# Performance work log

Hardware: AMD Instinct MI355X
Metric: run time of the kernel (lower is better)

Reference implementation:

```python
import jax, jax.numpy as jnp
import numpy as np

TAU = 10.0 / 7.0
V_TH = 1.0
ALPHA = 10.0  # sigmoid surrogate slope

@jax.custom_vjp
def spike_fn(v):
    # Heaviside(v - v_th) forward, sigmoid surrogate backward
    return (v >= V_TH).astype(v.dtype)

def _spike_fwd(v):
    return spike_fn(v), v

def _spike_bwd(v, g):
    s = jax.nn.sigmoid(ALPHA * (v - V_TH))
    return (g * ALPHA * s * (1.0 - s),)

spike_fn.defvjp(_spike_fwd, _spike_bwd)

def lif_multistep(x_bctm):
    # x: [B, C, T, M]; LIF recurrence over T axis, v_reset=0 hard reset,
    # decay_input=True: v = v + (x - v)/tau
    x_t = jnp.moveaxis(x_bctm, 2, 0)  # [T, B, C, M]
    def step(v, x):
        v = v + (x - v) / TAU
        s = spike_fn(v)
        v = v * (1.0 - s)  # hard reset to 0 (not detached)
        return v, s
    v0 = jnp.zeros_like(x_t[0])
    _, s_t = jax.lax.scan(step, v0, x_t)
    return jnp.moveaxis(s_t, 0, 2)  # [B, C, T, M]

def conv2d(x, w, pad, dil):
    return jax.lax.conv_general_dilated(
        x, w, window_strides=(1, 1),
        padding=[(pad[0], pad[0]), (pad[1], pad[1])],
        rhs_dilation=dil,
        dimension_numbers=('NCHW', 'OIHW', 'NCHW'))

def setup_inputs() -> dict:
    key = jax.random.key(0)
    k0, k1, k2, k3, k4 = jax.random.split(key, 5)
    B, T, M = 32, 128, 40
    x = jax.random.normal(k0, (B, 1, T, M), dtype=jnp.float32)
    # kaiming-ish init: std = 1/sqrt(fan_in)
    w1 = jax.random.normal(k1, (64, 1, 4, 3), dtype=jnp.float32) / np.sqrt(1 * 4 * 3)
    w2 = jax.random.normal(k2, (64, 64, 4, 3), dtype=jnp.float32) / np.sqrt(64 * 4 * 3)
    w3 = jax.random.normal(k3, (64, 64, 4, 3), dtype=jnp.float32) / np.sqrt(64 * 4 * 3)
    kw, kb = jax.random.split(k4)
    wf = jax.random.normal(kw, (12, 64 * 40), dtype=jnp.float32) / np.sqrt(64 * 40)
    bf = jnp.zeros((12,), dtype=jnp.float32)
    return {"x": x, "w1": w1, "w2": w2, "w3": w3, "wf": wf, "bf": bf}

def reference(x, w1, w2, w3, wf, bf):
    h = conv2d(x, w1, (2, 1), (1, 1))     # [B,64,T+1,40]
    h = lif_multistep(h)
    h = conv2d(h, w2, (6, 3), (4, 3))     # shape preserved
    h = lif_multistep(h)
    h = conv2d(h, w3, (24, 9), (16, 9))   # shape preserved
    h = lif_multistep(h)
    B, C, T, M = h.shape
    h = jnp.transpose(h, (0, 2, 1, 3)).reshape(B, T, C * M)  # flatten=True path
    y = h @ wf.T + bf                     # [B, T, 12]
    return y.mean(axis=1)                 # [B, 12]
```

## Files before the change

kernel.cpp:

```cpp
#include <hip/hip_runtime.h>


typedef __attribute__((ext_vector_type(8))) _Float16 v8h;
typedef __attribute__((ext_vector_type(16))) float v16f;
typedef __attribute__((ext_vector_type(4))) unsigned int u32x4;
typedef _Float16 half_t;

#define NB 32
#define NC 64
#define NT 129
#define TIN 128
#define NM 40
#define MS8 72
#define ROWB8 2952
#define SROWB8 2560

__global__ void prep_conv1(const float* __restrict__ w2s, const float* __restrict__ w3s,
                           uint4* __restrict__ wf2o, uint4* __restrict__ wf3o,
                           const float* __restrict__ x, const float* __restrict__ w1,
                           unsigned char* __restrict__ s1) {
    const int bx = blockIdx.x;
    if (bx < 96) {
        const float* w = (bx < 48) ? w2s : w3s;
        uint4* wf = (bx < 48) ? wf2o : wf3o;
        int tid = (bx % 48) * 256 + threadIdx.x;
        int lane = tid & 63;
        int rest = tid >> 6;
        int hl = rest & 1;
        int ct = (rest >> 1) & 1;
        int cq = (rest >> 2) & 3;
        int tap = rest >> 4;
        int kh = tap / 3, kw = tap % 3;
        int co = ct * 32 + (lane & 31);
        unsigned short o[8];
#pragma unroll
        for (int jj = 0; jj < 8; jj++) {
            int ci = cq * 16 + (lane >> 5) * 8 + jj;
            float wv = w[((co * 64 + ci) * 4 + kh) * 3 + kw];
            _Float16 hi = (_Float16)wv;
            _Float16 val = hl ? (_Float16)((wv - (float)hi) * 2048.0f) : hi;
            unsigned short us;
            __builtin_memcpy(&us, &val, 2);
            o[jj] = us;
        }
        uint4 r;
        __builtin_memcpy(&r, o, 16);
        wf[tid] = r;
        return;
    }
    const int idx = bx - 96;
    const int mg = idx % 10;
    const int b = idx / 10;
    const int c = threadIdx.x & 63;
    const int ml = threadIdx.x >> 6;
    const int m = mg * 4 + ml;
    float w[4][3];
#pragma unroll
    for (int kh = 0; kh < 4; kh++)
#pragma unroll
        for (int kw = 0; kw < 3; kw++) w[kh][kw] = w1[(c * 4 + kh) * 3 + kw];
    const float* xb = x + (size_t)b * TIN * NM;

    float xw[12][3];
#pragma unroll
    for (int rr = 0; rr < 12; rr++)
#pragma unroll
        for (int kw = 0; kw < 3; kw++) xw[rr][kw] = 0.f;
#pragma unroll
    for (int rr = 2; rr < 4; rr++)
#pragma unroll
        for (int kw = 0; kw < 3; kw++) {
            int mc = m - 1 + kw;
            xw[rr][kw] = ((unsigned)mc < (unsigned)NM) ? xb[(rr - 2) * NM + mc] : 0.f;
        }

    unsigned char* orow = s1 + ((size_t)b * NT * NM + m) * 64 + c;
    float v = 0.f;
    const float TAUc = 10.0f / 7.0f;

    for (int tb = 0; tb < NT; tb += 8) {
#pragma unroll
        for (int q = 0; q < 8; q++) {
            int row = tb + 2 + q;
#pragma unroll
            for (int kw = 0; kw < 3; kw++) {
                int mc = m - 1 + kw;
                xw[4 + q][kw] = (row < TIN && (unsigned)mc < (unsigned)NM)
                                    ? xb[row * NM + mc] : 0.f;
            }
        }
        int kmax = (NT - tb) < 8 ? (NT - tb) : 8;
#pragma unroll
        for (int k = 0; k < 8; k++) {
            if (k < kmax) {
                float uacc = 0.f;
#pragma unroll
                for (int kh = 0; kh < 4; kh++)
#pragma unroll
                    for (int kw = 0; kw < 3; kw++) uacc += xw[k + kh][kw] * w[kh][kw];
                v = v + (uacc - v) / TAUc;
                orow[(size_t)(tb + k) * NM * 64] = (v >= 1.0f) ? 1 : 0;
                if (v >= 1.0f) v = 0.0f;
            }
        }
#pragma unroll
        for (int rr = 0; rr < 4; rr++)
#pragma unroll
            for (int kw = 0; kw < 3; kw++) xw[rr][kw] = xw[8 + rr][kw];
    }
}

__device__ inline unsigned mul3c00(unsigned x) {
    unsigned r;
    asm("v_mul_u32_u24 %0, 0x3C00, %1" : "=v"(r) : "v"(x));
    return r;
}

__device__ inline v8h expand01(uint2 raw) {
    unsigned o0 = mul3c00(__builtin_amdgcn_perm(0u, raw.x, 0x04010400u));
    unsigned o1 = mul3c00(__builtin_amdgcn_perm(0u, raw.x, 0x04030402u));
    unsigned o2 = mul3c00(__builtin_amdgcn_perm(0u, raw.y, 0x04010400u));
    unsigned o3 = mul3c00(__builtin_amdgcn_perm(0u, raw.y, 0x04030402u));
    uint4 o = make_uint4(o0, o1, o2, o3);
    return __builtin_bit_cast(v8h, o);
}

template <int DH, int PH, int DW, int PW, int RMOD>
__global__ __launch_bounds__(256, 2) void convW(const unsigned char* __restrict__ spk,
                                                const uint4* __restrict__ wfrag,
                                                float* __restrict__ u) {
    __shared__ uint2 ldsq[7 * ROWB8 / 8];
    char* lds = (char*)ldsq;
    const int tid = threadIdx.x;
    const int lane = tid & 63;
    const int wv = tid >> 6;
    const int wp = wv >> 1;
    const int hl = wv & 1;
    const int bx = blockIdx.x;
    const int b = blockIdx.y;
    int r, jj0;
    if (bx < 32) { r = bx % RMOD; jj0 = (bx / RMOD) * 4; }
    else         { r = 0;         jj0 = (32 / RMOD) * 4; }

    const char* spb = (const char*)spk + (size_t)b * NT * SROWB8;
#pragma unroll
    for (int k = 0; k < 9; k++) {
        int c = tid + k * 256;
        if (c < 2296) {
            int i = c / 328;
            int rem = c - i * 328;
            int s = rem >> 3;
            int q = rem & 7;
            int tg = r - PH + DH * (jj0 + i);
            uint2 val = make_uint2(0u, 0u);
            if ((unsigned)tg < (unsigned)NT && s < 40)
                val = *(const uint2*)(spb + ((size_t)tg * NM + s) * 64 + q * 8);
            *(uint2*)(lds + i * ROWB8 + s * MS8 + q * 8) = val;
        }
    }

    const int pos = lane & 31;
    const int jl = pos >> 4;
    const int ml = pos & 15;
    const int hseg = lane >> 5;
    const int jj = jj0 + 2 * wp + jl;
    const int ldsrow = 2 * wp + jl;
    const int t = r + DH * jj;
    const int mtb[3] = {0, 16, 24};

    int P[3][3];
#pragma unroll
    for (int mt = 0; mt < 3; mt++)
#pragma unroll
        for (int kw = 0; kw < 3; kw++) {
            int md = mtb[mt] + ml + kw * DW - PW;
            int sel = ((unsigned)md < 40u) ? md : 40;
            P[mt][kw] = ldsrow * ROWB8 + sel * MS8 + hseg * 8;
        }

    v16f acc[3][2];
#pragma unroll
    for (int a = 0; a < 3; a++)
#pragma unroll
        for (int c2 = 0; c2 < 2; c2++) acc[a][c2] = (v16f)(0.0f);

    unsigned voff0 = (unsigned)(hl * 1024 + lane * 16);
    unsigned voff1 = voff0 + 4096u;
    const char* wbp = (const char*)wfrag;
    u32x4 Ab[2][4];

#define ISSUE4(PAR)                                                                   \
    {                                                                                 \
        asm volatile("global_load_dwordx4 %0, %1, %2"                                 \
                     : "=v"(Ab[PAR][0]) : "v"(voff0), "s"(wbp));                      \
        asm volatile("global_load_dwordx4 %0, %1, %2 offset:2048"                     \
                     : "=v"(Ab[PAR][1]) : "v"(voff0), "s"(wbp));                      \
        asm volatile("global_load_dwordx4 %0, %1, %2"                                 \
                     : "=v"(Ab[PAR][2]) : "v"(voff1), "s"(wbp));                      \
        asm volatile("global_load_dwordx4 %0, %1, %2 offset:2048"                     \
                     : "=v"(Ab[PAR][3]) : "v"(voff1), "s"(wbp));                      \
        wbp += 8192;                                                                  \
    }

    ISSUE4(0);
    __syncthreads();

#pragma unroll
    for (int s = 0; s < 24; ++s) {
        const int tap = s >> 1;
        const int kh = tap / 3, kw = tap % 3;
        if (s < 23) {
            if ((s & 1) == 0) ISSUE4(1) else ISSUE4(0);
            asm volatile("s_waitcnt vmcnt(4)");
        } else {
            asm volatile("s_waitcnt vmcnt(0)");
        }
        __builtin_amdgcn_sched_barrier(0);
#pragma unroll
        for (int j = 0; j < 2; ++j) {
            const int cq = (s & 1) * 2 + j;
            uint2 r0 = *(const uint2*)(lds + P[0][kw] + kh * ROWB8 + cq * 16);
            uint2 r1 = *(const uint2*)(lds + P[1][kw] + kh * ROWB8 + cq * 16);
            uint2 r2 = *(const uint2*)(lds + P[2][kw] + kh * ROWB8 + cq * 16);
            v8h B0 = expand01(r0);
            v8h B1 = expand01(r1);
            v8h B2 = expand01(r2);
            v8h A0 = __builtin_bit_cast(v8h, Ab[s & 1][j * 2 + 0]);
            v8h A1 = __builtin_bit_cast(v8h, Ab[s & 1][j * 2 + 1]);
            acc[0][0] = __builtin_amdgcn_mfma_f32_32x32x16_f16(A0, B0, acc[0][0], 0, 0, 0);
            acc[0][1] = __builtin_amdgcn_mfma_f32_32x32x16_f16(A1, B0, acc[0][1], 0, 0, 0);
            acc[1][0] = __builtin_amdgcn_mfma_f32_32x32x16_f16(A0, B1, acc[1][0], 0, 0, 0);
            acc[1][1] = __builtin_amdgcn_mfma_f32_32x32x16_f16(A1, B1, acc[1][1], 0, 0, 0);
            acc[2][0] = __builtin_amdgcn_mfma_f32_32x32x16_f16(A0, B2, acc[2][0], 0, 0, 0);
            acc[2][1] = __builtin_amdgcn_mfma_f32_32x32x16_f16(A1, B2, acc[2][1], 0, 0, 0);
        }
    }
#undef ISSUE4

    const float invs = 1.0f / 2048.0f;
    float4* lred = (float4*)lds;
    __syncthreads();
#pragma unroll
    for (int mt = 0; mt < 3; mt++) {
        if (hl) {
#pragma unroll
            for (int ct = 0; ct < 2; ct++)
#pragma unroll
                for (int g = 0; g < 4; g++) {
                    float4 vv;
                    vv.x = acc[mt][ct][4 * g + 0];
                    vv.y = acc[mt][ct][4 * g + 1];
                    vv.z = acc[mt][ct][4 * g + 2];
                    vv.w = acc[mt][ct][4 * g + 3];
                    lred[(wp * 8 + ct * 4 + g) * 64 + lane] = vv;
                }
        }
        __syncthreads();
        if (!hl && t < NT) {
            int m = mtb[mt] + ml;
            float* base = u + ((size_t)(b * NT + t) * NM + m) * 64;
#pragma unroll
            for (int ct = 0; ct < 2; ct++)
#pragma unroll
                for (int g = 0; g < 4; g++) {
                    float4 lo = lred[(wp * 8 + ct * 4 + g) * 64 + lane];
                    int co = ct * 32 + 8 * g + 4 * hseg;
                    float4 val;
                    val.x = acc[mt][ct][4 * g + 0] + lo.x * invs;
                    val.y = acc[mt][ct][4 * g + 1] + lo.y * invs;
                    val.z = acc[mt][ct][4 * g + 2] + lo.z * invs;
                    val.w = acc[mt][ct][4 * g + 3] + lo.w * invs;
                    *(float4*)(base + co) = val;
                }
        }
        __syncthreads();
    }
}

__global__ void lif_spikes(const float* __restrict__ u, unsigned char* __restrict__ s2) {
    int tid = blockIdx.x * 256 + threadIdx.x;
    int b = tid / 2560;
    int cm = tid % 2560;
    const float* up = u + (size_t)b * NT * 2560 + cm;
    unsigned char* sp = s2 + (size_t)b * NT * 2560 + cm;
    float v = 0.f;
    const float TAUc = 10.0f / 7.0f;
    for (int tb = 0; tb < 128; tb += 16) {
        float uu[16];
#pragma unroll
        for (int k = 0; k < 16; k++) uu[k] = up[(size_t)(tb + k) * 2560];
#pragma unroll
        for (int k = 0; k < 16; k++) {
            v = v + (uu[k] - v) / TAUc;
            sp[(size_t)(tb + k) * 2560] = (v >= 1.0f) ? 1 : 0;
            if (v >= 1.0f) v = 0.f;
        }
    }
    float uu = up[(size_t)128 * 2560];
    v = v + (uu - v) / TAUc;
    sp[(size_t)128 * 2560] = (v >= 1.0f) ? 1 : 0;
}

__global__ void lif_sum(const float* __restrict__ u, float* __restrict__ hsum) {
    int tid = blockIdx.x * 256 + threadIdx.x;
    int b = tid / 2560;
    int cm = tid % 2560;
    int m = cm >> 6;
    int co = cm & 63;
    const float* up = u + (size_t)b * NT * 2560 + cm;
    float v = 0.f, cnt = 0.f;
    const float TAUc = 10.0f / 7.0f;
    for (int tb = 0; tb < 128; tb += 16) {
        float uu[16];
#pragma unroll
        for (int k = 0; k < 16; k++) uu[k] = up[(size_t)(tb + k) * 2560];
#pragma unroll
        for (int k = 0; k < 16; k++) {
            v = v + (uu[k] - v) / TAUc;
            if (v >= 1.0f) { cnt += 1.0f; v = 0.f; }
        }
    }
    float uu = up[(size_t)128 * 2560];
    v = v + (uu - v) / TAUc;
    if (v >= 1.0f) cnt += 1.0f;
    hsum[b * 2560 + co * NM + m] = cnt;
}

__global__ void fc_out(const float* __restrict__ hsum, const float* __restrict__ wf,
                       const float* __restrict__ bfv, float* __restrict__ out) {
    int b = blockIdx.x;
    int tid = threadIdx.x;
    float p[12];
#pragma unroll
    for (int k = 0; k < 12; k++) p[k] = 0.0f;
    for (int cm = tid; cm < NC * NM; cm += 256) {
        float h = hsum[b * NC * NM + cm];
#pragma unroll
        for (int k = 0; k < 12; k++) p[k] += h * wf[k * (NC * NM) + cm];
    }
    __shared__ float red[12][4];
    int lane = tid & 63, w = tid >> 6;
#pragma unroll
    for (int k = 0; k < 12; k++) {
        float s = p[k];
#pragma unroll
        for (int off = 32; off > 0; off >>= 1) s += __shfl_down(s, off, 64);
        if (lane == 0) red[k][w] = s;
    }
    __syncthreads();
    if (tid < 12) {
        float s = red[tid][0] + red[tid][1] + red[tid][2] + red[tid][3];
        out[b * 12 + tid] = bfv[tid] + s / 129.0f;
    }
}

extern "C" void kernel_launch(void* const* d_in, const int* in_sizes, int n_in,
                              void* d_out, int out_size, void* d_ws, size_t ws_size,
                              hipStream_t stream) {
    const float* x  = (const float*)d_in[0];
    const float* w1 = (const float*)d_in[1];
    const float* w2 = (const float*)d_in[2];
    const float* w3 = (const float*)d_in[3];
    const float* wf = (const float*)d_in[4];
    const float* bf = (const float*)d_in[5];
    float* out = (float*)d_out;

    char* ws = (char*)d_ws;
    unsigned char* s1 = (unsigned char*)ws;
    unsigned char* s2 = (unsigned char*)(ws + 10567680);
    float*  u   = (float*)(ws + 21135360);
    uint4*  wf2 = (uint4*)(ws + 63406080);
    uint4*  wf3 = (uint4*)(ws + 63602688);
    float* hsum = (float*)(ws + 63799296);

    prep_conv1<<<416, 256, 0, stream>>>(w2, w3, wf2, wf3, x, w1, s1);

    convW<4, 6, 3, 3, 4><<<dim3(33, 32), 256, 0, stream>>>(s1, wf2, u);
    lif_spikes<<<320, 256, 0, stream>>>(u, s2);

    convW<16, 24, 9, 9, 16><<<dim3(33, 32), 256, 0, stream>>>(s2, wf3, u);
    lif_sum<<<320, 256, 0, stream>>>(u, hsum);

    fc_out<<<32, 256, 0, stream>>>(hsum, wf, bf, out);
}
```

Baseline: 201.8 us.

## Split conv work across output-channel halves per wave, doubling block count

Each block now covers two output time rows instead of four. The four waves are split by output-channel half (32 channels each) and by input-channel half, instead of by row pair. Per-wave accumulators shrink from six to three MFMA tiles, LDS use drops from 7 to 5 rows, and launch bounds rise to 4 blocks per CU, with twice as many blocks in the grid. The aim is higher occupancy and better load balance. In exchange, the spike-row halo is reloaded more often relative to the work done, and each B fragment is reused by fewer MFMAs.

```diff
diff --git a/kernel.cpp b/kernel.cpp
--- a/kernel.cpp
+++ b/kernel.cpp
@@ -126,27 +126,27 @@
 }
 
 template <int DH, int PH, int DW, int PW, int RMOD>
-__global__ __launch_bounds__(256, 2) void convW(const unsigned char* __restrict__ spk,
+__global__ __launch_bounds__(256, 4) void convW(const unsigned char* __restrict__ spk,
                                                 const uint4* __restrict__ wfrag,
                                                 float* __restrict__ u) {
-    __shared__ uint2 ldsq[7 * ROWB8 / 8];
+    __shared__ uint2 ldsq[5 * ROWB8 / 8];
     char* lds = (char*)ldsq;
     const int tid = threadIdx.x;
     const int lane = tid & 63;
     const int wv = tid >> 6;
-    const int wp = wv >> 1;
+    const int ct = wv >> 1;
     const int hl = wv & 1;
     const int bx = blockIdx.x;
     const int b = blockIdx.y;
     int r, jj0;
-    if (bx < 32) { r = bx % RMOD; jj0 = (bx / RMOD) * 4; }
-    else         { r = 0;         jj0 = (32 / RMOD) * 4; }
+    if (bx < 64) { r = bx % RMOD; jj0 = (bx / RMOD) * 2; }
+    else         { r = 0;         jj0 = (64 / RMOD) * 2; }
 
     const char* spb = (const char*)spk + (size_t)b * NT * SROWB8;
 #pragma unroll
-    for (int k = 0; k < 9; k++) {
+    for (int k = 0; k < 7; k++) {
         int c = tid + k * 256;
-        if (c < 2296) {
+        if (c < 1640) {
             int i = c / 328;
             int rem = c - i * 328;
             int s = rem >> 3;
@@ -163,8 +163,8 @@
     const int jl = pos >> 4;
     const int ml = pos & 15;
     const int hseg = lane >> 5;
-    const int jj = jj0 + 2 * wp + jl;
-    const int ldsrow = 2 * wp + jl;
+    const int jj = jj0 + jl;
+    const int ldsrow = jl;
     const int t = r + DH * jj;
     const int mtb[3] = {0, 16, 24};
 
@@ -178,31 +178,25 @@
             P[mt][kw] = ldsrow * ROWB8 + sel * MS8 + hseg * 8;
         }
 
-    v16f acc[3][2];
-#pragma unroll
-    for (int a = 0; a < 3; a++)
-#pragma unroll
-        for (int c2 = 0; c2 < 2; c2++) acc[a][c2] = (v16f)(0.0f);
-
-    unsigned voff0 = (unsigned)(hl * 1024 + lane * 16);
+    v16f acc[3];
+#pragma unroll
+    for (int a = 0; a < 3; a++) acc[a] = (v16f)(0.0f);
+
+    unsigned voff0 = (unsigned)(ct * 2048 + hl * 1024 + lane * 16);
     unsigned voff1 = voff0 + 4096u;
     const char* wbp = (const char*)wfrag;
-    u32x4 Ab[2][4];
-
-#define ISSUE4(PAR)                                                                   \
+    u32x4 Ab[2][2];
+
+#define ISSUE2(PAR)                                                                   \
     {                                                                                 \
         asm volatile("global_load_dwordx4 %0, %1, %2"                                 \
                      : "=v"(Ab[PAR][0]) : "v"(voff0), "s"(wbp));                      \
-        asm volatile("global_load_dwordx4 %0, %1, %2 offset:2048"                     \
-                     : "=v"(Ab[PAR][1]) : "v"(voff0), "s"(wbp));                      \
         asm volatile("global_load_dwordx4 %0, %1, %2"                                 \
-                     : "=v"(Ab[PAR][2]) : "v"(voff1), "s"(wbp));                      \
-        asm volatile("global_load_dwordx4 %0, %1, %2 offset:2048"                     \
-                     : "=v"(Ab[PAR][3]) : "v"(voff1), "s"(wbp));                      \
+                     : "=v"(Ab[PAR][1]) : "v"(voff1), "s"(wbp));                      \
         wbp += 8192;                                                                  \
     }
 
-    ISSUE4(0);
+    ISSUE2(0);
     __syncthreads();
 
 #pragma unroll
@@ -210,8 +204,8 @@
         const int tap = s >> 1;
         const int kh = tap / 3, kw = tap % 3;
         if (s < 23) {
-            if ((s & 1) == 0) ISSUE4(1) else ISSUE4(0);
-            asm volatile("s_waitcnt vmcnt(4)");
+            if ((s & 1) == 0) ISSUE2(1) else ISSUE2(0);
+            asm volatile("s_waitcnt vmcnt(2)");
         } else {
             asm volatile("s_waitcnt vmcnt(0)");
         }
@@ -225,17 +219,13 @@
             v8h B0 = expand01(r0);
             v8h B1 = expand01(r1);
             v8h B2 = expand01(r2);
-            v8h A0 = __builtin_bit_cast(v8h, Ab[s & 1][j * 2 + 0]);
-            v8h A1 = __builtin_bit_cast(v8h, Ab[s & 1][j * 2 + 1]);
-            acc[0][0] = __builtin_amdgcn_mfma_f32_32x32x16_f16(A0, B0, acc[0][0], 0, 0, 0);
-            acc[0][1] = __builtin_amdgcn_mfma_f32_32x32x16_f16(A1, B0, acc[0][1], 0, 0, 0);
-            acc[1][0] = __builtin_amdgcn_mfma_f32_32x32x16_f16(A0, B1, acc[1][0], 0, 0, 0);
-            acc[1][1] = __builtin_amdgcn_mfma_f32_32x32x16_f16(A1, B1, acc[1][1], 0, 0, 0);
-            acc[2][0] = __builtin_amdgcn_mfma_f32_32x32x16_f16(A0, B2, acc[2][0], 0, 0, 0);
-            acc[2][1] = __builtin_amdgcn_mfma_f32_32x32x16_f16(A1, B2, acc[2][1], 0, 0, 0);
-        }
-    }
-#undef ISSUE4
+            v8h A = __builtin_bit_cast(v8h, Ab[s & 1][j]);
+            acc[0] = __builtin_amdgcn_mfma_f32_32x32x16_f16(A, B0, acc[0], 0, 0, 0);
+            acc[1] = __builtin_amdgcn_mfma_f32_32x32x16_f16(A, B1, acc[1], 0, 0, 0);
+            acc[2] = __builtin_amdgcn_mfma_f32_32x32x16_f16(A, B2, acc[2], 0, 0, 0);
+        }
+    }
+#undef ISSUE2
 
     const float invs = 1.0f / 2048.0f;
     float4* lred = (float4*)lds;
@@ -244,34 +234,30 @@
     for (int mt = 0; mt < 3; mt++) {
         if (hl) {
 #pragma unroll
-            for (int ct = 0; ct < 2; ct++)
-#pragma unroll
-                for (int g = 0; g < 4; g++) {
-                    float4 vv;
-                    vv.x = acc[mt][ct][4 * g + 0];
-                    vv.y = acc[mt][ct][4 * g + 1];
-                    vv.z = acc[mt][ct][4 * g + 2];
-                    vv.w = acc[mt][ct][4 * g + 3];
-                    lred[(wp * 8 + ct * 4 + g) * 64 + lane] = vv;
-                }
+            for (int g = 0; g < 4; g++) {
+                float4 vv;
+                vv.x = acc[mt][4 * g + 0];
+                vv.y = acc[mt][4 * g + 1];
+                vv.z = acc[mt][4 * g + 2];
+                vv.w = acc[mt][4 * g + 3];
+                lred[(ct * 4 + g) * 64 + lane] = vv;
+            }
         }
         __syncthreads();
         if (!hl && t < NT) {
             int m = mtb[mt] + ml;
             float* base = u + ((size_t)(b * NT + t) * NM + m) * 64;
 #pragma unroll
-            for (int ct = 0; ct < 2; ct++)
-#pragma unroll
-                for (int g = 0; g < 4; g++) {
-                    float4 lo = lred[(wp * 8 + ct * 4 + g) * 64 + lane];
-                    int co = ct * 32 + 8 * g + 4 * hseg;
-                    float4 val;
-                    val.x = acc[mt][ct][4 * g + 0] + lo.x * invs;
-                    val.y = acc[mt][ct][4 * g + 1] + lo.y * invs;
-                    val.z = acc[mt][ct][4 * g + 2] + lo.z * invs;
-                    val.w = acc[mt][ct][4 * g + 3] + lo.w * invs;
-                    *(float4*)(base + co) = val;
-                }
+            for (int g = 0; g < 4; g++) {
+                float4 lo = lred[(ct * 4 + g) * 64 + lane];
+                int co = ct * 32 + 8 * g + 4 * hseg;
+                float4 val;
+                val.x = acc[mt][4 * g + 0] + lo.x * invs;
+                val.y = acc[mt][4 * g + 1] + lo.y * invs;
+                val.z = acc[mt][4 * g + 2] + lo.z * invs;
+                val.w = acc[mt][4 * g + 3] + lo.w * invs;
+                *(float4*)(base + co) = val;
+            }
         }
         __syncthreads();
     }
@@ -375,10 +361,10 @@
 
     prep_conv1<<<416, 256, 0, stream>>>(w2, w3, wf2, wf3, x, w1, s1);
 
-    convW<4, 6, 3, 3, 4><<<dim3(33, 32), 256, 0, stream>>>(s1, wf2, u);
+    convW<4, 6, 3, 3, 4><<<dim3(65, 32), 256, 0, stream>>>(s1, wf2, u);
     lif_spikes<<<320, 256, 0, stream>>>(u, s2);
 
-    convW<16, 24, 9, 9, 16><<<dim3(33, 32), 256, 0, stream>>>(s2, wf3, u);
+    convW<16, 24, 9, 9, 16><<<dim3(65, 32), 256, 0, stream>>>(s2, wf3, u);
     lif_sum<<<320, 256, 0, stream>>>(u, hsum);
 
     fc_out<<<32, 256, 0, stream>>>(hsum, wf, bf, out);
```

After: 203.8 us. No clear change (+1.0%).
